# Kernel optimization log

Measured on AMD Instinct MI355X. Metric: run time of the kernel, lower is better.

The kernel has to match this reference:

```python
import jax, jax.numpy as jnp
import numpy as np

N, L, S, H, E, D = 4, 1024, 1024, 16, 64, 64

def setup_inputs() -> dict:
    key = jax.random.key(0)
    kq, kk, kv = jax.random.split(key, 3)
    return {
        "queries": jax.random.normal(kq, (N, L, H, E), dtype=jnp.float32),
        "keys": jax.random.normal(kk, (N, S, H, E), dtype=jnp.float32),
        "values": jax.random.normal(kv, (N, S, H, D), dtype=jnp.float32),
        "attn_mask_add": jnp.zeros((L, S), dtype=jnp.float32),
        "key_lengths_add": jnp.zeros((N, S), dtype=jnp.float32),
    }

def reference(queries, keys, values, attn_mask_add, key_lengths_add):
    E_dim = queries.shape[-1]
    softmax_temp = 1.0 / jnp.sqrt(jnp.float32(E_dim))
    # scores: [N, H, L, S]
    QK = jnp.einsum('nlhe,nshe->nhls', queries, keys)
    QK = QK + attn_mask_add[None, None, :, :]
    QK = QK + key_lengths_add[:, None, None, :]
    A = jax.nn.softmax(softmax_temp * QK, axis=-1)  # dropout disabled (p=0)
    V = jnp.einsum('nhls,nshd->nlhd', A, values)
    return V
```

## Files before the change

kernel.cpp:

```cpp
#include <hip/hip_runtime.h>

typedef _Float16 f16x8  __attribute__((ext_vector_type(8)));
typedef _Float16 f16x4  __attribute__((ext_vector_type(4)));
typedef __fp16   hf2    __attribute__((ext_vector_type(2)));
typedef float    f32x4  __attribute__((ext_vector_type(4)));
typedef float    f32x16 __attribute__((ext_vector_type(16)));

namespace {
constexpr int kN = 4, kL = 1024, kS = 1024, kH = 16, kE = 64, kD = 64;
constexpr int kRowF = kH * kE;
constexpr int KVB = 64;
constexpr int NCH = kS / KVB;
constexpr float SCL = 0.125f * 1.44269504088896340736f;
}

__device__ __forceinline__ unsigned pku(float a, float b) {
  union { hf2 h; unsigned u; } u;
  u.h = __builtin_amdgcn_cvt_pkrtz(a, b);
  return u.u;
}
__device__ __forceinline__ f16x4 pk4(float a, float b, float c, float d) {
  union { hf2 h2[2]; f16x4 v; } u;
  u.h2[0] = __builtin_amdgcn_cvt_pkrtz(a, b);
  u.h2[1] = __builtin_amdgcn_cvt_pkrtz(c, d);
  return u.v;
}
__device__ __forceinline__ float xmax32(float t) {
  union { float f; unsigned u; } tu; tu.f = t;
  auto P = __builtin_amdgcn_permlane32_swap(tu.u, tu.u, false, false);
  union { unsigned u; float f; } a, b; a.u = P[0]; b.u = P[1];
  return fmaxf(a.f, b.f);
}
__device__ __forceinline__ float xsum32(float t) {
  union { float f; unsigned u; } tu; tu.f = t;
  auto P = __builtin_amdgcn_permlane32_swap(tu.u, tu.u, false, false);
  union { unsigned u; float f; } a, b; a.u = P[0]; b.u = P[1];
  return a.f + b.f;
}

__global__ __launch_bounds__(256)
void flag_kernel(const float* __restrict__ M, const float* __restrict__ KLN,
                 unsigned* __restrict__ F)
{
  constexpr size_t nM = (size_t)kL * kS / 4, nK = (size_t)kN * kS / 4;
  unsigned any = 0;
  for (size_t i = (size_t)blockIdx.x * 256 + threadIdx.x; i < nM + nK;
       i += (size_t)gridDim.x * 256) {
    const f32x4 v = (i < nM) ? reinterpret_cast<const f32x4*>(M)[i]
                             : reinterpret_cast<const f32x4*>(KLN)[i - nM];
    #pragma unroll
    for (int r = 0; r < 4; ++r)
      any |= (__float_as_uint(v[r]) << 1);
  }
  if (__any(any != 0) && (threadIdx.x & 63) == 0) atomicOr(F, 1u);
}

__global__ __launch_bounds__(512, 1)
void attn_fwd_kernel(const float* __restrict__ Q, const float* __restrict__ K,
                     const float* __restrict__ V, const float* __restrict__ M,
                     const float* __restrict__ KLN, float* __restrict__ O,
                     const unsigned* __restrict__ F)
{
  __shared__ _Float16 Ks[2][KVB * 64];
  __shared__ _Float16 Vt[2][kD * 64];

  const int tid  = threadIdx.x;
  const int lane = tid & 63;
  const int wave = tid >> 6;
  const int l31  = lane & 31;
  const int hi   = lane >> 5;
  const bool kRole = (wave < 4);
  const int srow = (tid >> 4) & 15;
  const int scol = tid & 15;

  const int useMask = F ? (int)F[0] : 1;

  const int swz = ((blockIdx.x & 7) << 5) | (blockIdx.x >> 3);
  const int nh = swz >> 2, qb = swz & 3;
  const int h = nh & (kH - 1), n = nh >> 4;
  const int qrow = qb * 256 + wave * 32 + l31;

  const float* Kp = K + ((size_t)n * kS * kH + h) * kE;
  const float* Vp = V + ((size_t)n * kS * kH + h) * kD;
  const float* Lp = KLN + (size_t)n * kS;
  const float* Mp = M + (size_t)qrow * kS;

  f16x8 qf[4];
  {
    const float* Qp = Q + ((size_t)((size_t)n * kL + qrow) * kH + h) * kE;
    #pragma unroll
    for (int ec = 0; ec < 4; ++ec) {
      const f32x4 a = *reinterpret_cast<const f32x4*>(Qp + 16*ec + 8*hi);
      const f32x4 b = *reinterpret_cast<const f32x4*>(Qp + 16*ec + 8*hi + 4);
      union { f16x4 h4[2]; f16x8 v; } u;
      u.h4[0] = pk4(a[0]*SCL, a[1]*SCL, a[2]*SCL, a[3]*SCL);
      u.h4[1] = pk4(b[0]*SCL, b[1]*SCL, b[2]*SCL, b[3]*SCL);
      qf[ec] = u.v;
    }
  }

  const int kxor = (l31 & 7) << 1;
  int keyv[2], vrowb[2];
  #pragma unroll
  for (int dt = 0; dt < 2; ++dt) {
    const int d = 32*dt + l31;
    keyv[dt] = ((4*((d>>2)&3) + (d&3)) ^ (d>>2)) & 15;
    vrowb[dt] = d * 64;
  }
  int hwv[4];
  #pragma unroll
  for (int jd = 0; jd < 4; ++jd)
    hwv[jd] = ((4*(scol & 3) + jd) ^ scol) & 15;

  const f32x16 z16 = {0,0,0,0, 0,0,0,0, 0,0,0,0, 0,0,0,0};
  f32x16 accA[2] = {z16, z16}, accB[2] = {z16, z16};
  float mA = -1e30f, lA = 0.f, mB = -1e30f, lB = 0.f;

  f32x4 sg[4];
  auto load_kv = [&](int sbase) {
    if (kRole) {
      #pragma unroll
      for (int i = 0; i < 4; ++i)
        sg[i] = *reinterpret_cast<const f32x4*>(Kp + (size_t)(sbase + 16*i + srow) * kRowF + 4*scol);
    } else {
      #pragma unroll
      for (int js = 0; js < 4; ++js)
        sg[js] = *reinterpret_cast<const f32x4*>(Vp + (size_t)(sbase + 4*srow + js) * kRowF + 4*scol);
    }
  };
  auto kv_write = [&](int buf) {
    if (kRole) {
      #pragma unroll
      for (int i = 0; i < 4; ++i) {
        const int s = 16*i + srow;
        *reinterpret_cast<f16x4*>(&Ks[buf][s*64 + ((scol ^ ((s & 7) << 1)) << 2)]) =
            pk4(sg[i][0], sg[i][1], sg[i][2], sg[i][3]);
      }
    } else {
      #pragma unroll
      for (int jd = 0; jd < 4; ++jd) {
        const int d = 4*scol + jd;
        *reinterpret_cast<f16x4*>(&Vt[buf][d*64 + ((srow ^ hwv[jd]) << 2)]) =
            pk4(sg[0][jd], sg[1][jd], sg[2][jd], sg[3][jd]);
      }
    }
  };

  auto half_tail = [&](const f32x16& cc, int hf, int s0h, float& mrun,
                       float& lsum, f32x16* acc) {
    float x[16];
    if (useMask) {
      #pragma unroll
      for (int m = 0; m < 4; ++m) {
        const f32x4 mv = *reinterpret_cast<const f32x4*>(Mp + s0h + 8*m + 4*hi);
        const f32x4 lv = *reinterpret_cast<const f32x4*>(Lp + s0h + 8*m + 4*hi);
        #pragma unroll
        for (int r = 0; r < 4; ++r)
          x[4*m+r] = fmaf(mv[r] + lv[r], SCL, cc[4*m+r]);
      }
    } else {
      #pragma unroll
      for (int r = 0; r < 16; ++r) x[r] = cc[r];
    }
    float mx[8];
    #pragma unroll
    for (int i = 0; i < 8; ++i) mx[i] = fmaxf(x[i], x[i+8]);
    #pragma unroll
    for (int w = 4; w >= 1; w >>= 1)
      #pragma unroll
      for (int i = 0; i < w; ++i) mx[i] = fmaxf(mx[i], mx[i+w]);
    const float tmax = xmax32(mx[0]);

    if (!__all(tmax <= mrun + 8.f)) {
      const float mnew = fmaxf(mrun, tmax);
      const float rs = __builtin_amdgcn_exp2f(mrun - mnew);
      mrun = mnew; lsum *= rs;
      acc[0] *= rs; acc[1] *= rs;
    }
    #pragma unroll
    for (int i = 0; i < 16; ++i)
      x[i] = __builtin_amdgcn_exp2f(x[i] - mrun);
    float s8[8];
    #pragma unroll
    for (int i = 0; i < 8; ++i) s8[i] = x[i] + x[i+8];
    #pragma unroll
    for (int w = 4; w >= 1; w >>= 1)
      #pragma unroll
      for (int i = 0; i < w; ++i) s8[i] += s8[i+w];
    lsum += s8[0];

    f16x8 pf[2];
    #pragma unroll
    for (int sc = 0; sc < 2; ++sc) {
      const int b = sc * 8;
      const unsigned k0 = pku(x[b+0], x[b+1]);
      const unsigned k1 = pku(x[b+2], x[b+3]);
      const unsigned w0 = pku(x[b+4], x[b+5]);
      const unsigned w1 = pku(x[b+6], x[b+7]);
      auto X = __builtin_amdgcn_permlane32_swap(k0, w0, false, false);
      auto Y = __builtin_amdgcn_permlane32_swap(k1, w1, false, false);
      union { unsigned u[4]; f16x8 v; } pu;
      pu.u[0] = X[0]; pu.u[1] = Y[0]; pu.u[2] = X[1]; pu.u[3] = Y[1];
      pf[sc] = pu.v;
    }
    const int cur = (s0h / KVB) & 1;
    __builtin_amdgcn_s_setprio(1);
    #pragma unroll
    for (int dt = 0; dt < 2; ++dt) {
      #pragma unroll
      for (int sc = 0; sc < 2; ++sc) {
        const int scg = hf*2 + sc;
        const int sl0 = ((scg << 2) + (hi << 1)) ^ keyv[dt];
        union { f16x4 h4[2]; f16x8 v; } vu;
        vu.h4[0] = *reinterpret_cast<const f16x4*>(&Vt[cur][vrowb[dt] + (sl0 << 2)]);
        vu.h4[1] = *reinterpret_cast<const f16x4*>(&Vt[cur][vrowb[dt] + ((sl0 ^ 1) << 2)]);
        acc[dt] = __builtin_amdgcn_mfma_f32_32x32x16_f16(vu.v, pf[sc], acc[dt], 0, 0, 0);
      }
    }
    __builtin_amdgcn_s_setprio(0);
  };

  load_kv(0);
  kv_write(0);
  load_kv(KVB);

  for (int c = 0; c < NCH; ++c) {
    const int cur = c & 1;
    const int s0 = c * KVB;
    __syncthreads();
    if (c + 1 < NCH) kv_write(cur ^ 1);
    if (c + 2 < NCH) load_kv((c + 2) * KVB);

    f32x16 ccA = z16, ccB = z16;
    __builtin_amdgcn_s_setprio(1);
    #pragma unroll
    for (int ec = 0; ec < 4; ++ec) {
      const f16x8 kfA = *reinterpret_cast<const f16x8*>(
          &Ks[cur][l31*64 + ((((ec << 2) + (hi << 1)) ^ kxor) << 2)]);
      ccA = __builtin_amdgcn_mfma_f32_32x32x16_f16(kfA, qf[ec], ccA, 0, 0, 0);
    }
    #pragma unroll
    for (int ec = 0; ec < 4; ++ec) {
      const f16x8 kfB = *reinterpret_cast<const f16x8*>(
          &Ks[cur][l31*64 + 2048 + ((((ec << 2) + (hi << 1)) ^ kxor) << 2)]);
      ccB = __builtin_amdgcn_mfma_f32_32x32x16_f16(kfB, qf[ec], ccB, 0, 0, 0);
    }
    __builtin_amdgcn_s_setprio(0);

    half_tail(ccA, 0, s0,      mA, lA, accA);
    half_tail(ccB, 1, s0 + 32, mB, lB, accB);
  }

  lA = xsum32(lA);
  lB = xsum32(lB);
  const float mM = fmaxf(mA, mB);
  const float wA = __builtin_amdgcn_exp2f(mA - mM);
  const float wB = __builtin_amdgcn_exp2f(mB - mM);
  const float inv = 1.f / (lA * wA + lB * wB);
  float* Op = O + (((size_t)n * kL + qrow) * kH + h) * kD;
  #pragma unroll
  for (int dt = 0; dt < 2; ++dt)
    #pragma unroll
    for (int m = 0; m < 4; ++m) {
      f32x4 o;
      #pragma unroll
      for (int r = 0; r < 4; ++r)
        o[r] = (accA[dt][4*m+r] * wA + accB[dt][4*m+r] * wB) * inv;
      *reinterpret_cast<f32x4*>(Op + 32*dt + 8*m + 4*hi) = o;
    }
}

extern "C" void kernel_launch(void* const* d_in, const int* in_sizes, int n_in,
                              void* d_out, int out_size, void* d_ws, size_t ws_size,
                              hipStream_t stream) {
  const float* Q   = (const float*)d_in[0];
  const float* K   = (const float*)d_in[1];
  const float* V   = (const float*)d_in[2];
  const float* M   = (const float*)d_in[3];
  const float* KLN = (const float*)d_in[4];
  float* O = (float*)d_out;

  unsigned* F = nullptr;
  if (ws_size >= sizeof(unsigned)) {
    F = (unsigned*)d_ws;
    hipMemsetAsync(F, 0, sizeof(unsigned), stream);
    flag_kernel<<<dim3(1024), dim3(256), 0, stream>>>(M, KLN, F);
  }

  dim3 grid(kN * kH * (kL / 256));
  dim3 block(512);
  attn_fwd_kernel<<<grid, block, 0, stream>>>(Q, K, V, M, KLN, O, F);
}
```

Baseline: 54.13 us.

## Switch attention to 16x16 MFMA tiles with 128-row query blocks

Restructures the attention kernel so each wave owns 16 query rows and uses 16x16x32 and 16x16x16 f16 MFMAs instead of 32x32x16. A single online-softmax state per lane replaces the two per-half states. The block now covers 128 queries instead of 256, which doubles the grid, and the launch bounds allow several blocks per CU to raise occupancy and latency hiding. In exchange, each K/V chunk is staged through shared memory for half as many queries, so K/V global traffic and conversion work double.

```diff
diff --git a/kernel.cpp b/kernel.cpp
--- a/kernel.cpp
+++ b/kernel.cpp
@@ -4,7 +4,6 @@
 typedef _Float16 f16x4  __attribute__((ext_vector_type(4)));
 typedef __fp16   hf2    __attribute__((ext_vector_type(2)));
 typedef float    f32x4  __attribute__((ext_vector_type(4)));
-typedef float    f32x16 __attribute__((ext_vector_type(16)));
 
 namespace {
 constexpr int kN = 4, kL = 1024, kS = 1024, kH = 16, kE = 64, kD = 64;
@@ -14,11 +13,6 @@
 constexpr float SCL = 0.125f * 1.44269504088896340736f;
 }
 
-__device__ __forceinline__ unsigned pku(float a, float b) {
-  union { hf2 h; unsigned u; } u;
-  u.h = __builtin_amdgcn_cvt_pkrtz(a, b);
-  return u.u;
-}
 __device__ __forceinline__ f16x4 pk4(float a, float b, float c, float d) {
   union { hf2 h2[2]; f16x4 v; } u;
   u.h2[0] = __builtin_amdgcn_cvt_pkrtz(a, b);
@@ -55,7 +49,7 @@
   if (__any(any != 0) && (threadIdx.x & 63) == 0) atomicOr(F, 1u);
 }
 
-__global__ __launch_bounds__(512, 1)
+__global__ __launch_bounds__(512, 4)
 void attn_fwd_kernel(const float* __restrict__ Q, const float* __restrict__ K,
                      const float* __restrict__ V, const float* __restrict__ M,
                      const float* __restrict__ KLN, float* __restrict__ O,
@@ -67,54 +61,55 @@
   const int tid  = threadIdx.x;
   const int lane = tid & 63;
   const int wave = tid >> 6;
-  const int l31  = lane & 31;
-  const int hi   = lane >> 5;
+  const int qc   = lane & 15;
+  const int g    = lane >> 4;
   const bool kRole = (wave < 4);
-  const int srow = (tid >> 4) & 15;
-  const int scol = tid & 15;
+  const int stid = tid & 255;
+  const int srow = stid >> 4;
+  const int scol = stid & 15;
 
   const int useMask = F ? (int)F[0] : 1;
 
-  const int swz = ((blockIdx.x & 7) << 5) | (blockIdx.x >> 3);
-  const int nh = swz >> 2, qb = swz & 3;
+  const int swz = ((blockIdx.x & 7) << 6) | (blockIdx.x >> 3);
+  const int nh = swz >> 3, qb = swz & 7;
   const int h = nh & (kH - 1), n = nh >> 4;
-  const int qrow = qb * 256 + wave * 32 + l31;
+  const int qrow = qb * 128 + wave * 16 + qc;
 
   const float* Kp = K + ((size_t)n * kS * kH + h) * kE;
   const float* Vp = V + ((size_t)n * kS * kH + h) * kD;
   const float* Lp = KLN + (size_t)n * kS;
   const float* Mp = M + (size_t)qrow * kS;
 
-  f16x8 qf[4];
+  f16x8 qf0, qf1;
   {
     const float* Qp = Q + ((size_t)((size_t)n * kL + qrow) * kH + h) * kE;
-    #pragma unroll
-    for (int ec = 0; ec < 4; ++ec) {
-      const f32x4 a = *reinterpret_cast<const f32x4*>(Qp + 16*ec + 8*hi);
-      const f32x4 b = *reinterpret_cast<const f32x4*>(Qp + 16*ec + 8*hi + 4);
-      union { f16x4 h4[2]; f16x8 v; } u;
-      u.h4[0] = pk4(a[0]*SCL, a[1]*SCL, a[2]*SCL, a[3]*SCL);
-      u.h4[1] = pk4(b[0]*SCL, b[1]*SCL, b[2]*SCL, b[3]*SCL);
-      qf[ec] = u.v;
-    }
-  }
-
-  const int kxor = (l31 & 7) << 1;
-  int keyv[2], vrowb[2];
+    const f32x4 a0 = *reinterpret_cast<const f32x4*>(Qp + 8*g);
+    const f32x4 b0 = *reinterpret_cast<const f32x4*>(Qp + 8*g + 4);
+    const f32x4 a1 = *reinterpret_cast<const f32x4*>(Qp + 32 + 8*g);
+    const f32x4 b1 = *reinterpret_cast<const f32x4*>(Qp + 32 + 8*g + 4);
+    union { f16x4 h4[2]; f16x8 v; } u0, u1;
+    u0.h4[0] = pk4(a0[0]*SCL, a0[1]*SCL, a0[2]*SCL, a0[3]*SCL);
+    u0.h4[1] = pk4(b0[0]*SCL, b0[1]*SCL, b0[2]*SCL, b0[3]*SCL);
+    u1.h4[0] = pk4(a1[0]*SCL, a1[1]*SCL, a1[2]*SCL, a1[3]*SCL);
+    u1.h4[1] = pk4(b1[0]*SCL, b1[1]*SCL, b1[2]*SCL, b1[3]*SCL);
+    qf0 = u0.v; qf1 = u1.v;
+  }
+
+  const int koff = qc*64 + ((g ^ (qc & 7)) << 3);
+  int hv[4], vrow[4];
   #pragma unroll
-  for (int dt = 0; dt < 2; ++dt) {
-    const int d = 32*dt + l31;
-    keyv[dt] = ((4*((d>>2)&3) + (d&3)) ^ (d>>2)) & 15;
-    vrowb[dt] = d * 64;
+  for (int t = 0; t < 4; ++t) {
+    hv[t] = (qc ^ (4*t + (qc >> 2))) & 15;
+    vrow[t] = (16*t + qc) * 64;
   }
   int hwv[4];
   #pragma unroll
   for (int jd = 0; jd < 4; ++jd)
     hwv[jd] = ((4*(scol & 3) + jd) ^ scol) & 15;
 
-  const f32x16 z16 = {0,0,0,0, 0,0,0,0, 0,0,0,0, 0,0,0,0};
-  f32x16 accA[2] = {z16, z16}, accB[2] = {z16, z16};
-  float mA = -1e30f, lA = 0.f, mB = -1e30f, lB = 0.f;
+  const f32x4 z4 = {0.f, 0.f, 0.f, 0.f};
+  f32x4 acc[4] = {z4, z4, z4, z4};
+  float mrun = -1e30f, lsum = 0.f;
 
   f32x4 sg[4];
   auto load_kv = [&](int sbase) {
@@ -144,80 +139,6 @@
             pk4(sg[0][jd], sg[1][jd], sg[2][jd], sg[3][jd]);
       }
     }
-  };
-
-  auto half_tail = [&](const f32x16& cc, int hf, int s0h, float& mrun,
-                       float& lsum, f32x16* acc) {
-    float x[16];
-    if (useMask) {
-      #pragma unroll
-      for (int m = 0; m < 4; ++m) {
-        const f32x4 mv = *reinterpret_cast<const f32x4*>(Mp + s0h + 8*m + 4*hi);
-        const f32x4 lv = *reinterpret_cast<const f32x4*>(Lp + s0h + 8*m + 4*hi);
-        #pragma unroll
-        for (int r = 0; r < 4; ++r)
-          x[4*m+r] = fmaf(mv[r] + lv[r], SCL, cc[4*m+r]);
-      }
-    } else {
-      #pragma unroll
-      for (int r = 0; r < 16; ++r) x[r] = cc[r];
-    }
-    float mx[8];
-    #pragma unroll
-    for (int i = 0; i < 8; ++i) mx[i] = fmaxf(x[i], x[i+8]);
-    #pragma unroll
-    for (int w = 4; w >= 1; w >>= 1)
-      #pragma unroll
-      for (int i = 0; i < w; ++i) mx[i] = fmaxf(mx[i], mx[i+w]);
-    const float tmax = xmax32(mx[0]);
-
-    if (!__all(tmax <= mrun + 8.f)) {
-      const float mnew = fmaxf(mrun, tmax);
-      const float rs = __builtin_amdgcn_exp2f(mrun - mnew);
-      mrun = mnew; lsum *= rs;
-      acc[0] *= rs; acc[1] *= rs;
-    }
-    #pragma unroll
-    for (int i = 0; i < 16; ++i)
-      x[i] = __builtin_amdgcn_exp2f(x[i] - mrun);
-    float s8[8];
-    #pragma unroll
-    for (int i = 0; i < 8; ++i) s8[i] = x[i] + x[i+8];
-    #pragma unroll
-    for (int w = 4; w >= 1; w >>= 1)
-      #pragma unroll
-      for (int i = 0; i < w; ++i) s8[i] += s8[i+w];
-    lsum += s8[0];
-
-    f16x8 pf[2];
-    #pragma unroll
-    for (int sc = 0; sc < 2; ++sc) {
-      const int b = sc * 8;
-      const unsigned k0 = pku(x[b+0], x[b+1]);
-      const unsigned k1 = pku(x[b+2], x[b+3]);
-      const unsigned w0 = pku(x[b+4], x[b+5]);
-      const unsigned w1 = pku(x[b+6], x[b+7]);
-      auto X = __builtin_amdgcn_permlane32_swap(k0, w0, false, false);
-      auto Y = __builtin_amdgcn_permlane32_swap(k1, w1, false, false);
-      union { unsigned u[4]; f16x8 v; } pu;
-      pu.u[0] = X[0]; pu.u[1] = Y[0]; pu.u[2] = X[1]; pu.u[3] = Y[1];
-      pf[sc] = pu.v;
-    }
-    const int cur = (s0h / KVB) & 1;
-    __builtin_amdgcn_s_setprio(1);
-    #pragma unroll
-    for (int dt = 0; dt < 2; ++dt) {
-      #pragma unroll
-      for (int sc = 0; sc < 2; ++sc) {
-        const int scg = hf*2 + sc;
-        const int sl0 = ((scg << 2) + (hi << 1)) ^ keyv[dt];
-        union { f16x4 h4[2]; f16x8 v; } vu;
-        vu.h4[0] = *reinterpret_cast<const f16x4*>(&Vt[cur][vrowb[dt] + (sl0 << 2)]);
-        vu.h4[1] = *reinterpret_cast<const f16x4*>(&Vt[cur][vrowb[dt] + ((sl0 ^ 1) << 2)]);
-        acc[dt] = __builtin_amdgcn_mfma_f32_32x32x16_f16(vu.v, pf[sc], acc[dt], 0, 0, 0);
-      }
-    }
-    __builtin_amdgcn_s_setprio(0);
   };
 
   load_kv(0);
@@ -231,43 +152,96 @@
     if (c + 1 < NCH) kv_write(cur ^ 1);
     if (c + 2 < NCH) load_kv((c + 2) * KVB);
 
-    f32x16 ccA = z16, ccB = z16;
+    f32x4 cc[4];
     __builtin_amdgcn_s_setprio(1);
     #pragma unroll
-    for (int ec = 0; ec < 4; ++ec) {
-      const f16x8 kfA = *reinterpret_cast<const f16x8*>(
-          &Ks[cur][l31*64 + ((((ec << 2) + (hi << 1)) ^ kxor) << 2)]);
-      ccA = __builtin_amdgcn_mfma_f32_32x32x16_f16(kfA, qf[ec], ccA, 0, 0, 0);
-    }
-    #pragma unroll
-    for (int ec = 0; ec < 4; ++ec) {
-      const f16x8 kfB = *reinterpret_cast<const f16x8*>(
-          &Ks[cur][l31*64 + 2048 + ((((ec << 2) + (hi << 1)) ^ kxor) << 2)]);
-      ccB = __builtin_amdgcn_mfma_f32_32x32x16_f16(kfB, qf[ec], ccB, 0, 0, 0);
+    for (int st = 0; st < 4; ++st) {
+      const f16x8 kf0 = *reinterpret_cast<const f16x8*>(&Ks[cur][st*1024 + koff]);
+      const f16x8 kf1 = *reinterpret_cast<const f16x8*>(&Ks[cur][st*1024 + (koff ^ 32)]);
+      f32x4 t = z4;
+      t = __builtin_amdgcn_mfma_f32_16x16x32_f16(kf0, qf0, t, 0, 0, 0);
+      t = __builtin_amdgcn_mfma_f32_16x16x32_f16(kf1, qf1, t, 0, 0, 0);
+      cc[st] = t;
     }
     __builtin_amdgcn_s_setprio(0);
 
-    half_tail(ccA, 0, s0,      mA, lA, accA);
-    half_tail(ccB, 1, s0 + 32, mB, lB, accB);
-  }
-
-  lA = xsum32(lA);
-  lB = xsum32(lB);
-  const float mM = fmaxf(mA, mB);
-  const float wA = __builtin_amdgcn_exp2f(mA - mM);
-  const float wB = __builtin_amdgcn_exp2f(mB - mM);
-  const float inv = 1.f / (lA * wA + lB * wB);
+    float x[16];
+    if (useMask) {
+      #pragma unroll
+      for (int st = 0; st < 4; ++st) {
+        const f32x4 mv = *reinterpret_cast<const f32x4*>(Mp + s0 + st*16 + 4*g);
+        const f32x4 lv = *reinterpret_cast<const f32x4*>(Lp + s0 + st*16 + 4*g);
+        #pragma unroll
+        for (int r = 0; r < 4; ++r)
+          x[st*4+r] = fmaf(mv[r] + lv[r], SCL, cc[st][r]);
+      }
+    } else {
+      #pragma unroll
+      for (int st = 0; st < 4; ++st)
+        #pragma unroll
+        for (int r = 0; r < 4; ++r)
+          x[st*4+r] = cc[st][r];
+    }
+
+    float mx[8];
+    #pragma unroll
+    for (int i = 0; i < 8; ++i) mx[i] = fmaxf(x[i], x[i+8]);
+    #pragma unroll
+    for (int w = 4; w >= 1; w >>= 1)
+      #pragma unroll
+      for (int i = 0; i < w; ++i) mx[i] = fmaxf(mx[i], mx[i+w]);
+    float tmax = fmaxf(mx[0], __shfl_xor(mx[0], 16));
+    tmax = xmax32(tmax);
+
+    if (!__all(tmax <= mrun + 8.f)) {
+      const float mnew = fmaxf(mrun, tmax);
+      const float rs = __builtin_amdgcn_exp2f(mrun - mnew);
+      mrun = mnew; lsum *= rs;
+      acc[0] *= rs; acc[1] *= rs; acc[2] *= rs; acc[3] *= rs;
+    }
+    #pragma unroll
+    for (int i = 0; i < 16; ++i)
+      x[i] = __builtin_amdgcn_exp2f(x[i] - mrun);
+    float s8[8];
+    #pragma unroll
+    for (int i = 0; i < 8; ++i) s8[i] = x[i] + x[i+8];
+    #pragma unroll
+    for (int w = 4; w >= 1; w >>= 1)
+      #pragma unroll
+      for (int i = 0; i < w; ++i) s8[i] += s8[i+w];
+    lsum += s8[0];
+
+    f16x4 pb[4];
+    #pragma unroll
+    for (int st = 0; st < 4; ++st)
+      pb[st] = pk4(x[st*4+0], x[st*4+1], x[st*4+2], x[st*4+3]);
+
+    __builtin_amdgcn_s_setprio(1);
+    #pragma unroll
+    for (int t = 0; t < 4; ++t) {
+      #pragma unroll
+      for (int st = 0; st < 4; ++st) {
+        const int slot = ((4*st + g) ^ hv[t]) << 2;
+        const f16x4 vf = *reinterpret_cast<const f16x4*>(&Vt[cur][vrow[t] + slot]);
+        acc[t] = __builtin_amdgcn_mfma_f32_16x16x16f16(vf, pb[st], acc[t], 0, 0, 0);
+      }
+    }
+    __builtin_amdgcn_s_setprio(0);
+  }
+
+  lsum += __shfl_xor(lsum, 16);
+  lsum = xsum32(lsum);
+  const float inv = 1.f / lsum;
   float* Op = O + (((size_t)n * kL + qrow) * kH + h) * kD;
   #pragma unroll
-  for (int dt = 0; dt < 2; ++dt)
-    #pragma unroll
-    for (int m = 0; m < 4; ++m) {
-      f32x4 o;
-      #pragma unroll
-      for (int r = 0; r < 4; ++r)
-        o[r] = (accA[dt][4*m+r] * wA + accB[dt][4*m+r] * wB) * inv;
-      *reinterpret_cast<f32x4*>(Op + 32*dt + 8*m + 4*hi) = o;
-    }
+  for (int t = 0; t < 4; ++t) {
+    f32x4 o;
+    o[0] = acc[t][0] * inv;
+    o[1] = acc[t][1] * inv;
+    o[2] = acc[t][2] * inv;
+    o[3] = acc[t][3] * inv;
+    *reinterpret_cast<f32x4*>(Op + 16*t + 4*g) = o;
+  }
 }
 
 extern "C" void kernel_launch(void* const* d_in, const int* in_sizes, int n_in,
@@ -287,7 +261,7 @@
     flag_kernel<<<dim3(1024), dim3(256), 0, stream>>>(M, KLN, F);
   }
 
-  dim3 grid(kN * kH * (kL / 256));
+  dim3 grid(kN * kH * (kL / 128));
   dim3 block(512);
   attn_fwd_kernel<<<grid, block, 0, stream>>>(Q, K, V, M, KLN, O, F);
 }
```

New measurement: 49.96 us. -7.7%, faster.
